# Kernel tuning notes

Hardware: AMD Instinct MI355X
Metric: run time of the kernel (lower is better)

Reference implementation:

```python
import jax, jax.numpy as jnp
import numpy as np

B, S, D = 1, 2048, 2048
H, G, HD = 32, 8, 64
EPS = 1e-6
ROPE_BASE = 10000.0


def rms_norm(x, g):
    # torch RMSNorm computed in fp32 then cast back (PytorchRMSNorm wrapper)
    xf = x.astype(jnp.float32)
    y = xf * jax.lax.rsqrt(jnp.mean(xf * xf, axis=-1, keepdims=True) + EPS) * g.astype(jnp.float32)
    return y.astype(x.dtype)


def rotate_half(x):
    x1, x2 = jnp.split(x, 2, axis=-1)
    return jnp.concatenate([-x2, x1], axis=-1)


def apply_rope(x, cos, sin):
    # x: (b, h, s, hd); cos/sin: (s, hd)
    return x * cos[None, None] + rotate_half(x) * sin[None, None]


def setup_inputs() -> dict:
    key = jax.random.key(0)
    ks = jax.random.split(key, 8)
    x = jax.random.normal(ks[0], (B, S, D), dtype=jnp.float32)
    wq = jax.random.normal(ks[1], (H * HD, D), dtype=jnp.float32) * (D ** -0.5)
    wk = jax.random.normal(ks[2], (G * HD, D), dtype=jnp.float32) * (D ** -0.5)
    wv = jax.random.normal(ks[3], (G * HD, D), dtype=jnp.float32) * (D ** -0.5)
    wo = jax.random.normal(ks[4], (D, H * HD), dtype=jnp.float32) * (D ** -0.5)
    qg = jnp.ones((HD,), dtype=jnp.float32)
    kg = jnp.ones((HD,), dtype=jnp.float32)
    # RoPE tables (HF-style: duplicated half-dim frequencies)
    inv_freq = 1.0 / (ROPE_BASE ** (jnp.arange(0, HD, 2, dtype=jnp.float32) / HD))
    ang = jnp.arange(S, dtype=jnp.float32)[:, None] * inv_freq[None, :]  # (S, HD/2)
    emb = jnp.concatenate([ang, ang], axis=-1)  # (S, HD)
    cos = jnp.cos(emb)
    sin = jnp.sin(emb)
    # causal mask: True = future (upper-right triangle)
    mask = jnp.triu(jnp.ones((S, S), dtype=bool), k=1)
    return {"x": x, "mask": mask, "cos": cos, "sin": sin,
            "wq": wq, "wk": wk, "wv": wv, "wo": wo, "qg": qg, "kg": kg}


def reference(x, mask, cos, sin, wq, wk, wv, wo, qg, kg):
    b, s, _ = x.shape
    rep = H // G
    q = (x @ wq.T).reshape(b, s, H, HD).transpose(0, 2, 1, 3)   # (b,H,s,hd)
    k = (x @ wk.T).reshape(b, s, G, HD).transpose(0, 2, 1, 3)   # (b,G,s,hd)
    v = (x @ wv.T).reshape(b, s, G, HD).transpose(0, 2, 1, 3)
    q = rms_norm(q, qg)
    k = rms_norm(k, kg)
    q = apply_rope(q, cos[:s], sin[:s])
    k = apply_rope(k, cos[:s], sin[:s])
    k = jnp.repeat(k, rep, axis=1)  # (b,H,s,hd) GQA expansion
    v = jnp.repeat(v, rep, axis=1)
    scores = jnp.einsum('bhqd,bhkd->bhqk', q, k) * (HD ** -0.5)
    neg = jnp.finfo(scores.dtype).min / 2
    scores = jnp.where(mask[None, None, :s, :s], neg, scores)
    w = jax.nn.softmax(scores, axis=-1)
    ctx = jnp.einsum('bhqk,bhkd->bhqd', w, v)
    ctx = ctx.transpose(0, 2, 1, 3).reshape(b, s, H * HD)
    return ctx @ wo.T
```

## Files before the change

kernel.cpp:

```cpp
#include <hip/hip_runtime.h>
#include <stdint.h>

#define SEQ    2048
#define DMODEL 2048
#define NHEAD  32
#define NKV    8
#define HDIM   64
#define NQKV   3072

typedef __bf16 bf16x8 __attribute__((ext_vector_type(8)));
typedef float  f32x4  __attribute__((ext_vector_type(4)));

#define SCALE2 0.180336880f
#define THR2   12.0f

__device__ __forceinline__ ushort bf(float f){
  __bf16 h = (__bf16)f;
  return __builtin_bit_cast(unsigned short, h);
}
__device__ __forceinline__ float b2f(ushort v){
  union { uint32_t u; float f; } a; a.u = ((uint32_t)v) << 16; return a.f;
}
__device__ __forceinline__ float ex2(float x){
  return __builtin_amdgcn_exp2f(x);
}
__device__ __forceinline__ float fmax3(float a, float b, float c){
  float r;
  asm("v_max3_f32 %0, %1, %2, %3" : "=v"(r) : "v"(a), "v"(b), "v"(c));
  return r;
}

__device__ __forceinline__ void gl_lds16(const void* g, void* l){
  __builtin_amdgcn_global_load_lds(
      (const __attribute__((address_space(1))) uint32_t*)g,
      (__attribute__((address_space(3))) uint32_t*)l, 16, 0, 0);
}

__global__ __launch_bounds__(256) void k_cvt_all(const float* __restrict__ x,
                                                 const float* __restrict__ wq,
                                                 const float* __restrict__ wk,
                                                 const float* __restrict__ wv,
                                                 const float* __restrict__ wo,
                                                 ushort* __restrict__ xb,
                                                 ushort* __restrict__ wcat,
                                                 ushort* __restrict__ wob){
  int i = blockIdx.x * 256 + threadIdx.x;
  const float* src; ushort* dst; int s4; int d4;
  if (i < 1048576)      { src = x;  dst = xb;   s4 = i;           d4 = s4; }
  else if (i < 2097152) { src = wq; dst = wcat; s4 = i - 1048576; d4 = s4; }
  else if (i < 2359296) { src = wk; dst = wcat; s4 = i - 2097152; d4 = s4 + 1048576; }
  else if (i < 2621440) { src = wv; dst = wcat; s4 = i - 2359296; d4 = s4 + 1310720; }
  else                  { src = wo; dst = wob;  s4 = i - 2621440; d4 = s4; }
  float4 v = reinterpret_cast<const float4*>(src)[s4];
  ushort4 o;
  o.x = bf(v.x); o.y = bf(v.y); o.z = bf(v.z); o.w = bf(v.w);
  reinterpret_cast<ushort4*>(dst)[d4] = o;
}

__global__ __launch_bounds__(256) void k_gemm_bt(const ushort* __restrict__ A,
                                                 const ushort* __restrict__ B,
                                                 float* __restrict__ C,
                                                 int M, int N, int K){
  __shared__ ushort As[2][128*64];
  __shared__ ushort Bs[2][64*64];
  const int tid = threadIdx.x, lane = tid & 63, wid = tid >> 6;
  const int bm = blockIdx.y * 128, bn = blockIdx.x * 64;
  const int wr = wid >> 1, wc = wid & 1;
  const int l15 = lane & 15, u = lane >> 4;

  const int crow = lane >> 3;
  const int scol = ((lane & 7) ^ crow) * 8;
  const ushort* Abase = A + (size_t)(bm + wid*32 + crow) * K + scol;
  const ushort* Bbase = B + (size_t)(bn + wid*16 + crow) * K + scol;

  auto STAGE = [&](int buf, int k0){
#pragma unroll
    for (int c = 0; c < 4; c++)
      gl_lds16(Abase + k0 + (size_t)c*8*K, &As[buf][(wid*32 + c*8)*64]);
#pragma unroll
    for (int c = 0; c < 2; c++)
      gl_lds16(Bbase + k0 + (size_t)c*8*K, &Bs[buf][(wid*16 + c*8)*64]);
  };

  f32x4 acc[4][2] = {};
  const int NT = K >> 6;

  STAGE(0, 0);
  __syncthreads();

  for (int t = 0; t < NT; t++){
    const int cur = t & 1;
    if (t + 1 < NT) STAGE(cur ^ 1, (t + 1) << 6);

#pragma unroll
    for (int kc = 0; kc < 2; kc++){
      bf16x8 af[4], bfr[2];
#pragma unroll
      for (int m = 0; m < 4; m++){
        int row = wr*64 + m*16 + l15;
        af[m] = *reinterpret_cast<const bf16x8*>(&As[cur][row*64 + (((kc*4+u) ^ (row&7))*8)]);
      }
#pragma unroll
      for (int n = 0; n < 2; n++){
        int row = wc*32 + n*16 + l15;
        bfr[n] = *reinterpret_cast<const bf16x8*>(&Bs[cur][row*64 + (((kc*4+u) ^ (row&7))*8)]);
      }
      __builtin_amdgcn_s_setprio(1);
#pragma unroll
      for (int m = 0; m < 4; m++)
#pragma unroll
        for (int n = 0; n < 2; n++)
          acc[m][n] = __builtin_amdgcn_mfma_f32_16x16x32_bf16(af[m], bfr[n], acc[m][n], 0, 0, 0);
      __builtin_amdgcn_s_setprio(0);
    }

    __syncthreads();
  }

#pragma unroll
  for (int m = 0; m < 4; m++)
#pragma unroll
    for (int n = 0; n < 2; n++)
#pragma unroll
      for (int j = 0; j < 4; j++){
        int row = bm + wr*64 + m*16 + u*4 + j;
        int col = bn + wc*32 + n*16 + l15;
        C[(size_t)row * N + col] = acc[m][n][j];
      }
}

__global__ __launch_bounds__(256) void k_gemm_btc(const ushort* __restrict__ A,
                                                  const ushort* __restrict__ B,
                                                  ushort* __restrict__ C,
                                                  int M, int N, int K){
  __shared__ ushort As[2][128*64];
  __shared__ ushort Bs[2][96*64];
  const int tid = threadIdx.x, lane = tid & 63, wid = tid >> 6;
  const int bm = blockIdx.y * 128, bn = blockIdx.x * 96;
  const int wr = wid >> 1, wc = wid & 1;
  const int l15 = lane & 15, u = lane >> 4;

  const int crow = lane >> 3;
  const int scol = ((lane & 7) ^ crow) * 8;
  const ushort* Abase = A + (size_t)(bm + wid*32 + crow) * K + scol;
  const ushort* Bbase = B + (size_t)(bn + wid*24 + crow) * K + scol;

  auto STAGE = [&](int buf, int k0){
#pragma unroll
    for (int c = 0; c < 4; c++)
      gl_lds16(Abase + k0 + (size_t)c*8*K, &As[buf][(wid*32 + c*8)*64]);
#pragma unroll
    for (int c = 0; c < 3; c++)
      gl_lds16(Bbase + k0 + (size_t)c*8*K, &Bs[buf][(wid*24 + c*8)*64]);
  };

  f32x4 acc[4][3] = {};
  const int NT = K >> 6;

  STAGE(0, 0);
  __syncthreads();

  for (int t = 0; t < NT; t++){
    const int cur = t & 1;
    if (t + 1 < NT) STAGE(cur ^ 1, (t + 1) << 6);

#pragma unroll
    for (int kc = 0; kc < 2; kc++){
      bf16x8 af[4], bfr[3];
#pragma unroll
      for (int m = 0; m < 4; m++){
        int row = wr*64 + m*16 + l15;
        af[m] = *reinterpret_cast<const bf16x8*>(&As[cur][row*64 + (((kc*4+u) ^ (row&7))*8)]);
      }
#pragma unroll
      for (int n = 0; n < 3; n++){
        int row = wc*48 + n*16 + l15;
        bfr[n] = *reinterpret_cast<const bf16x8*>(&Bs[cur][row*64 + (((kc*4+u) ^ (row&7))*8)]);
      }
      __builtin_amdgcn_s_setprio(1);
#pragma unroll
      for (int m = 0; m < 4; m++)
#pragma unroll
        for (int n = 0; n < 3; n++)
          acc[m][n] = __builtin_amdgcn_mfma_f32_16x16x32_bf16(af[m], bfr[n], acc[m][n], 0, 0, 0);
      __builtin_amdgcn_s_setprio(0);
    }

    __syncthreads();
  }

#pragma unroll
  for (int m = 0; m < 4; m++)
#pragma unroll
    for (int n = 0; n < 3; n++)
#pragma unroll
      for (int j = 0; j < 4; j++){
        int row = bm + wr*64 + m*16 + u*4 + j;
        int col = bn + wc*48 + n*16 + l15;
        C[(size_t)row * N + col] = bf(acc[m][n][j]);
      }
}

__global__ __launch_bounds__(256) void k_normrope(const ushort* __restrict__ qkvc,
                                                  const float* __restrict__ cosp,
                                                  const float* __restrict__ sinp,
                                                  const float* __restrict__ qg,
                                                  const float* __restrict__ kg,
                                                  ushort* __restrict__ qb,
                                                  ushort* __restrict__ kb){
  const int s = blockIdx.x;
  const int tid = threadIdx.x, lane = tid & 63, wid = tid >> 6;
  const ushort* row = qkvc + (size_t)s * NQKV;
  const float cs = cosp[s*HDIM + lane];
  const float sn = sinp[s*HDIM + lane];

  for (int hidx = wid; hidx < 40; hidx += 4){
    const bool isq = hidx < 32;
    const int col = isq ? hidx*64 : 2048 + (hidx-32)*64;
    float x = b2f(row[col + lane]);
    float ss = x * x;
#pragma unroll
    for (int m = 1; m < 64; m <<= 1) ss += __shfl_xor(ss, m);
    float r = rsqrtf(ss * (1.0f/64.0f) + 1e-6f);
    float y = x * r * (isq ? qg : kg)[lane];
    float p = __shfl_xor(y, 32);
    float out = y * cs + (lane < 32 ? -p : p) * sn;
    if (isq) qb[(size_t)s*2048 + hidx*64 + lane] = bf(out * SCALE2);
    else     kb[(size_t)s*512 + (hidx-32)*64 + lane] = bf(out);
  }
}

__global__ __launch_bounds__(256) void k_vtrans(const ushort* __restrict__ qkvc,
                                                ushort* __restrict__ vtb){
  __shared__ ushort tile[64][68];
  const int g = blockIdx.x >> 5, st = blockIdx.x & 31;
  const int tid = threadIdx.x;
#pragma unroll
  for (int i = 0; i < 4; i++){
    int idx = i*256 + tid;
    int r = idx >> 4, c4 = idx & 15;
    ushort4 v = *reinterpret_cast<const ushort4*>(
        qkvc + (size_t)(st*64 + r)*NQKV + 2560 + g*64 + c4*4);
    tile[c4*4+0][r] = v.x;
    tile[c4*4+1][r] = v.y;
    tile[c4*4+2][r] = v.z;
    tile[c4*4+3][r] = v.w;
  }
  __syncthreads();
#pragma unroll
  for (int i = 0; i < 4; i++){
    int idx = i*256 + tid;
    int d = idx >> 4, s4 = idx & 15;
    int pos4 = (s4 >> 3)*32 + (s4 & 3)*8 + ((s4 >> 2) & 1)*4;
    ushort4 o = *reinterpret_cast<const ushort4*>(&tile[d][s4*4]);
    *reinterpret_cast<ushort4*>(vtb + (size_t)(g*64 + d)*SEQ + st*64 + pos4) = o;
  }
}

__global__ __launch_bounds__(256, 4) void k_attn(const ushort* __restrict__ qbuf,
                                                 const ushort* __restrict__ kbuf,
                                                 const ushort* __restrict__ vtb,
                                                 ushort* __restrict__ op,
                                                 float2* __restrict__ ml){
  __shared__ ushort Kd[2][64*64];
  __shared__ ushort Vd[2][64*64];

  const int bx = blockIdx.x;
  const int c = bx & 255, slot = bx >> 8;
  const int h = c >> 3, j = c & 7;
  const int qt   = (slot & 1) ? j : 15 - j;
  const int part = slot >> 1;
  const int g = h >> 2;
  const int t0 = part ? (qt + 1)   : 0;
  const int t1 = part ? (2*qt + 2) : (qt + 1);
  const int tid = threadIdx.x, lane = tid & 63, wid = tid >> 6;
  const int l15 = lane & 15, u = lane >> 4;
  const int q0 = qt*128 + wid*32;

  bf16x8 qf[2][2];
#pragma unroll
  for (int hh = 0; hh < 2; hh++)
#pragma unroll
    for (int kc = 0; kc < 2; kc++)
      qf[hh][kc] = *reinterpret_cast<const bf16x8*>(
          qbuf + (size_t)(q0 + hh*16 + l15)*2048 + h*64 + kc*32 + u*8);

  f32x4 o[2][4] = {};
  float mrun[2] = {-1e30f, -1e30f};
  float lrun[2] = {0.f, 0.f};

  int koff[8], voff[8];
#pragma unroll
  for (int kb = 0; kb < 4; kb++)
#pragma unroll
    for (int kc = 0; kc < 2; kc++){
      int keyl = kb*16 + l15;
      koff[kb*2+kc] = (keyl*64 + (((kc*4+u) ^ (keyl&7))*8)) * 2;
    }
#pragma unroll
  for (int kc = 0; kc < 2; kc++)
#pragma unroll
    for (int d0 = 0; d0 < 4; d0++){
      int vrow = d0*16 + l15;
      voff[kc*4+d0] = (vrow*64 + (((kc*4+u) ^ (vrow&7))*8)) * 2;
    }

  const int srow = wid*16 + (lane >> 3);
  const int scol = ((lane & 7) ^ (lane >> 3)) * 8;
  const ushort* ksrc0 = kbuf + (size_t)srow*512 + g*64 + scol;
  const ushort* vsrc0 = vtb  + (size_t)(g*64 + srow)*SEQ + scol;

  auto STAGE = [&](int buf, int t){
    const ushort* ks = ksrc0 + (size_t)t*64*512;
    gl_lds16(ks,         &Kd[buf][wid*1024]);
    gl_lds16(ks + 8*512, &Kd[buf][wid*1024 + 512]);
    const ushort* vs = vsrc0 + t*64;
    gl_lds16(vs,          &Vd[buf][wid*1024]);
    gl_lds16(vs + 8*SEQ,  &Vd[buf][wid*1024 + 512]);
  };

  STAGE(0, t0);
  __syncthreads();

  for (int t = t0; t < t1; t++){
    const int cur = (t - t0) & 1;
    if (t + 1 < t1) STAGE(cur ^ 1, t + 1);

    const char* KB = (const char*)Kd + cur*8192;
    const char* VB = (const char*)Vd + cur*8192;

    f32x4 st[2][4];
#pragma unroll
    for (int kb = 0; kb < 4; kb++){
      const int key0 = t*64 + kb*16;
      bf16x8 kf0 = *reinterpret_cast<const bf16x8*>(KB + koff[kb*2]);
      bf16x8 kf1 = *reinterpret_cast<const bf16x8*>(KB + koff[kb*2+1]);
#pragma unroll
      for (int hh = 0; hh < 2; hh++){
        if (key0 <= q0 + hh*16 + 15){
          f32x4 a = {};
          a = __builtin_amdgcn_mfma_f32_16x16x32_bf16(kf0, qf[hh][0], a, 0, 0, 0);
          a = __builtin_amdgcn_mfma_f32_16x16x32_bf16(kf1, qf[hh][1], a, 0, 0, 0);
          st[hh][kb] = a;
        } else {
          st[hh][kb] = (f32x4){-1e30f, -1e30f, -1e30f, -1e30f};
        }
      }
    }
#pragma unroll
    for (int hh = 0; hh < 2; hh++){
      if (!((t*64 + 63) <= q0 + hh*16)){
        const int keyb = t*64 + u*4;
        const int qr = q0 + hh*16 + l15;
#pragma unroll
        for (int kb = 0; kb < 4; kb++)
#pragma unroll
          for (int jj = 0; jj < 4; jj++)
            st[hh][kb][jj] = (keyb + kb*16 + jj > qr) ? -1e30f : st[hh][kb][jj];
      }
    }

#pragma unroll
    for (int hh = 0; hh < 2; hh++){
      float r0 = fmax3(st[hh][0][0], st[hh][0][1], st[hh][0][2]);
      float r1 = fmax3(st[hh][0][3], st[hh][1][0], st[hh][1][1]);
      float r2 = fmax3(st[hh][1][2], st[hh][1][3], st[hh][2][0]);
      float r3 = fmax3(st[hh][2][1], st[hh][2][2], st[hh][2][3]);
      float r4 = fmax3(st[hh][3][0], st[hh][3][1], st[hh][3][2]);
      float m0 = fmax3(r0, r1, r2);
      float m1 = fmax3(r3, r4, st[hh][3][3]);
      float tml = fmaxf(m0, m1);
      if (__any(tml > mrun[hh] + THR2)){
        float tm = fmaxf(tml, __shfl_xor(tml, 16));
        tm = fmaxf(tm, __shfl_xor(tm, 32));
        float mn = fmaxf(mrun[hh], tm);
        float al = ex2(mrun[hh] - mn);
        mrun[hh] = mn;
        lrun[hh] *= al;
#pragma unroll
        for (int d0 = 0; d0 < 4; d0++)
#pragma unroll
          for (int jj = 0; jj < 4; jj++) o[hh][d0][jj] *= al;
      }
      float ls[4];
#pragma unroll
      for (int kb = 0; kb < 4; kb++){
        float p0 = ex2(st[hh][kb][0] - mrun[hh]);
        float p1 = ex2(st[hh][kb][1] - mrun[hh]);
        float p2 = ex2(st[hh][kb][2] - mrun[hh]);
        float p3 = ex2(st[hh][kb][3] - mrun[hh]);
        st[hh][kb][0] = p0; st[hh][kb][1] = p1;
        st[hh][kb][2] = p2; st[hh][kb][3] = p3;
        ls[kb] = (p0 + p1) + (p2 + p3);
      }
      lrun[hh] += (ls[0] + ls[1]) + (ls[2] + ls[3]);
    }

    __builtin_amdgcn_s_setprio(1);
#pragma unroll
    for (int kc = 0; kc < 2; kc++){
      union { uint32_t w[4]; bf16x8 v; } pb[2];
#pragma unroll
      for (int hh = 0; hh < 2; hh++){
        asm("v_cvt_pk_bf16_f32 %0, %1, %2" : "=v"(pb[hh].w[0]) : "v"(st[hh][2*kc  ][0]), "v"(st[hh][2*kc  ][1]));
        asm("v_cvt_pk_bf16_f32 %0, %1, %2" : "=v"(pb[hh].w[1]) : "v"(st[hh][2*kc  ][2]), "v"(st[hh][2*kc  ][3]));
        asm("v_cvt_pk_bf16_f32 %0, %1, %2" : "=v"(pb[hh].w[2]) : "v"(st[hh][2*kc+1][0]), "v"(st[hh][2*kc+1][1]));
        asm("v_cvt_pk_bf16_f32 %0, %1, %2" : "=v"(pb[hh].w[3]) : "v"(st[hh][2*kc+1][2]), "v"(st[hh][2*kc+1][3]));
      }
#pragma unroll
      for (int d0 = 0; d0 < 4; d0++){
        bf16x8 vb8 = *reinterpret_cast<const bf16x8*>(VB + voff[kc*4+d0]);
        o[0][d0] = __builtin_amdgcn_mfma_f32_16x16x32_bf16(vb8, pb[0].v, o[0][d0], 0, 0, 0);
        o[1][d0] = __builtin_amdgcn_mfma_f32_16x16x32_bf16(vb8, pb[1].v, o[1][d0], 0, 0, 0);
      }
    }
    __builtin_amdgcn_s_setprio(0);

    __syncthreads();
  }

#pragma unroll
  for (int hh = 0; hh < 2; hh++){
    float lt = lrun[hh] + __shfl_xor(lrun[hh], 16);
    lt += __shfl_xor(lt, 32);
    float inv = lt > 0.f ? 1.0f / lt : 0.f;
    const size_t ridx = (size_t)part*65536 + h*2048 + (q0 + hh*16 + l15);
#pragma unroll
    for (int d0 = 0; d0 < 4; d0++){
      ushort4 w;
      w.x = bf(o[hh][d0][0] * inv); w.y = bf(o[hh][d0][1] * inv);
      w.z = bf(o[hh][d0][2] * inv); w.w = bf(o[hh][d0][3] * inv);
      *reinterpret_cast<ushort4*>(&op[ridx*64 + d0*16 + u*4]) = w;
    }
    if (lane < 16) ml[ridx] = make_float2(mrun[hh], lt);
  }
}

__global__ __launch_bounds__(256) void k_comb(const ushort* __restrict__ op,
                                              const float2* __restrict__ ml,
                                              ushort* __restrict__ ctx){
  const int tq = blockIdx.x*256 + threadIdx.x;
  const int q = tq & 3, row = (tq >> 2) & 2047, h = tq >> 13;
  const int idx = h*2048 + row;
  float2 a = ml[idx], b = ml[idx + 65536];
  float m = fmaxf(a.x, b.x);
  float w0 = ex2(a.x - m) * a.y;
  float w1 = ex2(b.x - m) * b.y;
  float inv = 1.0f / (w0 + w1);
  w0 *= inv; w1 *= inv;
  const ushort4* p0 = reinterpret_cast<const ushort4*>(op + (size_t)idx*64 + q*16);
  const ushort4* p1 = reinterpret_cast<const ushort4*>(op + ((size_t)idx + 65536)*64 + q*16);
  ushort* dst = ctx + (size_t)row*2048 + h*64 + q*16;
#pragma unroll
  for (int i = 0; i < 4; i++){
    ushort4 x0 = p0[i], x1 = p1[i];
    ushort4 w;
    w.x = bf(w0*b2f(x0.x) + w1*b2f(x1.x));
    w.y = bf(w0*b2f(x0.y) + w1*b2f(x1.y));
    w.z = bf(w0*b2f(x0.z) + w1*b2f(x1.z));
    w.w = bf(w0*b2f(x0.w) + w1*b2f(x1.w));
    reinterpret_cast<ushort4*>(dst)[i] = w;
  }
}

extern "C" void kernel_launch(void* const* d_in, const int* in_sizes, int n_in,
                              void* d_out, int out_size, void* d_ws, size_t ws_size,
                              hipStream_t stream){
  const float* x    = (const float*)d_in[0];
  const float* cosp = (const float*)d_in[2];
  const float* sinp = (const float*)d_in[3];
  const float* wq   = (const float*)d_in[4];
  const float* wk   = (const float*)d_in[5];
  const float* wv   = (const float*)d_in[6];
  const float* wo   = (const float*)d_in[7];
  const float* qg   = (const float*)d_in[8];
  const float* kg   = (const float*)d_in[9];
  float* out = (float*)d_out;

  char* ws = (char*)d_ws;
  ushort* xb   = (ushort*)(ws);
  ushort* wcat = (ushort*)(ws + 8388608);
  ushort* wob  = (ushort*)(ws + 20971520);
  ushort* qkvc = (ushort*)(ws + 29360128);
  ushort* qb   = (ushort*)(ws + 41943040);
  ushort* kb   = (ushort*)(ws + 50331648);
  ushort* vtb  = (ushort*)(ws + 52428800);
  ushort* ctxb = (ushort*)(ws + 54525952);
  ushort* op   = (ushort*)(ws);
  float2* ml   = (float2*)(ws + 16777216);

  k_cvt_all<<<14336, 256, 0, stream>>>(x, wq, wk, wv, wo, xb, wcat, wob);
  k_gemm_btc<<<dim3(32, 16), 256, 0, stream>>>(xb, wcat, qkvc, 2048, 3072, 2048);
  k_normrope<<<2048, 256, 0, stream>>>(qkvc, cosp, sinp, qg, kg, qb, kb);
  k_vtrans<<<256, 256, 0, stream>>>(qkvc, vtb);
  k_attn<<<1024, 256, 0, stream>>>(qb, kb, vtb, op, ml);
  k_comb<<<1024, 256, 0, stream>>>(op, ml, ctxb);
  k_gemm_bt<<<dim3(32, 16), 256, 0, stream>>>(ctxb, wob, out, 2048, 2048, 2048);
}
```

Baseline: 130.6 us.

## Merge norm-rope and V-transpose launches, raise QK MFMA priority, widen combine loads

```diff
diff --git a/kernel.cpp b/kernel.cpp
--- a/kernel.cpp
+++ b/kernel.cpp
@@ -10,6 +10,7 @@
 
 typedef __bf16 bf16x8 __attribute__((ext_vector_type(8)));
 typedef float  f32x4  __attribute__((ext_vector_type(4)));
+typedef unsigned short ushort8 __attribute__((ext_vector_type(8)));
 
 #define SCALE2 0.180336880f
 #define THR2   12.0f
@@ -201,59 +202,60 @@
       }
 }
 
-__global__ __launch_bounds__(256) void k_normrope(const ushort* __restrict__ qkvc,
-                                                  const float* __restrict__ cosp,
-                                                  const float* __restrict__ sinp,
-                                                  const float* __restrict__ qg,
-                                                  const float* __restrict__ kg,
-                                                  ushort* __restrict__ qb,
-                                                  ushort* __restrict__ kb){
-  const int s = blockIdx.x;
+__global__ __launch_bounds__(256) void k_prep(const ushort* __restrict__ qkvc,
+                                              const float* __restrict__ cosp,
+                                              const float* __restrict__ sinp,
+                                              const float* __restrict__ qg,
+                                              const float* __restrict__ kg,
+                                              ushort* __restrict__ qb,
+                                              ushort* __restrict__ kb,
+                                              ushort* __restrict__ vtb){
+  __shared__ ushort tile[64][68];
+  const int bx = blockIdx.x;
   const int tid = threadIdx.x, lane = tid & 63, wid = tid >> 6;
-  const ushort* row = qkvc + (size_t)s * NQKV;
-  const float cs = cosp[s*HDIM + lane];
-  const float sn = sinp[s*HDIM + lane];
-
-  for (int hidx = wid; hidx < 40; hidx += 4){
-    const bool isq = hidx < 32;
-    const int col = isq ? hidx*64 : 2048 + (hidx-32)*64;
-    float x = b2f(row[col + lane]);
-    float ss = x * x;
-#pragma unroll
-    for (int m = 1; m < 64; m <<= 1) ss += __shfl_xor(ss, m);
-    float r = rsqrtf(ss * (1.0f/64.0f) + 1e-6f);
-    float y = x * r * (isq ? qg : kg)[lane];
-    float p = __shfl_xor(y, 32);
-    float out = y * cs + (lane < 32 ? -p : p) * sn;
-    if (isq) qb[(size_t)s*2048 + hidx*64 + lane] = bf(out * SCALE2);
-    else     kb[(size_t)s*512 + (hidx-32)*64 + lane] = bf(out);
-  }
-}
-
-__global__ __launch_bounds__(256) void k_vtrans(const ushort* __restrict__ qkvc,
-                                                ushort* __restrict__ vtb){
-  __shared__ ushort tile[64][68];
-  const int g = blockIdx.x >> 5, st = blockIdx.x & 31;
-  const int tid = threadIdx.x;
-#pragma unroll
-  for (int i = 0; i < 4; i++){
-    int idx = i*256 + tid;
-    int r = idx >> 4, c4 = idx & 15;
-    ushort4 v = *reinterpret_cast<const ushort4*>(
-        qkvc + (size_t)(st*64 + r)*NQKV + 2560 + g*64 + c4*4);
-    tile[c4*4+0][r] = v.x;
-    tile[c4*4+1][r] = v.y;
-    tile[c4*4+2][r] = v.z;
-    tile[c4*4+3][r] = v.w;
-  }
-  __syncthreads();
-#pragma unroll
-  for (int i = 0; i < 4; i++){
-    int idx = i*256 + tid;
-    int d = idx >> 4, s4 = idx & 15;
-    int pos4 = (s4 >> 3)*32 + (s4 & 3)*8 + ((s4 >> 2) & 1)*4;
-    ushort4 o = *reinterpret_cast<const ushort4*>(&tile[d][s4*4]);
-    *reinterpret_cast<ushort4*>(vtb + (size_t)(g*64 + d)*SEQ + st*64 + pos4) = o;
+
+  if (bx < 2048){
+    const int s = bx;
+    const ushort* row = qkvc + (size_t)s * NQKV;
+    const float cs = cosp[s*HDIM + lane];
+    const float sn = sinp[s*HDIM + lane];
+    for (int hidx = wid; hidx < 40; hidx += 4){
+      const bool isq = hidx < 32;
+      const int col = isq ? hidx*64 : 2048 + (hidx-32)*64;
+      float x = b2f(row[col + lane]);
+      float ss = x * x;
+#pragma unroll
+      for (int m = 1; m < 64; m <<= 1) ss += __shfl_xor(ss, m);
+      float r = rsqrtf(ss * (1.0f/64.0f) + 1e-6f);
+      float y = x * r * (isq ? qg : kg)[lane];
+      float p = __shfl_xor(y, 32);
+      float out = y * cs + (lane < 32 ? -p : p) * sn;
+      if (isq) qb[(size_t)s*2048 + hidx*64 + lane] = bf(out * SCALE2);
+      else     kb[(size_t)s*512 + (hidx-32)*64 + lane] = bf(out);
+    }
+  } else {
+    const int b = bx - 2048;
+    const int g = b >> 5, st = b & 31;
+#pragma unroll
+    for (int i = 0; i < 4; i++){
+      int idx = i*256 + tid;
+      int r = idx >> 4, c4 = idx & 15;
+      ushort4 v = *reinterpret_cast<const ushort4*>(
+          qkvc + (size_t)(st*64 + r)*NQKV + 2560 + g*64 + c4*4);
+      tile[c4*4+0][r] = v.x;
+      tile[c4*4+1][r] = v.y;
+      tile[c4*4+2][r] = v.z;
+      tile[c4*4+3][r] = v.w;
+    }
+    __syncthreads();
+#pragma unroll
+    for (int i = 0; i < 4; i++){
+      int idx = i*256 + tid;
+      int d = idx >> 4, s4 = idx & 15;
+      int pos4 = (s4 >> 3)*32 + (s4 & 3)*8 + ((s4 >> 2) & 1)*4;
+      ushort4 o = *reinterpret_cast<const ushort4*>(&tile[d][s4*4]);
+      *reinterpret_cast<ushort4*>(vtb + (size_t)(g*64 + d)*SEQ + st*64 + pos4) = o;
+    }
   }
 }
 
@@ -330,6 +332,7 @@
     const char* VB = (const char*)Vd + cur*8192;
 
     f32x4 st[2][4];
+    __builtin_amdgcn_s_setprio(1);
 #pragma unroll
     for (int kb = 0; kb < 4; kb++){
       const int key0 = t*64 + kb*16;
@@ -347,6 +350,7 @@
         }
       }
     }
+    __builtin_amdgcn_s_setprio(0);
 #pragma unroll
     for (int hh = 0; hh < 2; hh++){
       if (!((t*64 + 63) <= q0 + hh*16)){
@@ -448,18 +452,17 @@
   float w1 = ex2(b.x - m) * b.y;
   float inv = 1.0f / (w0 + w1);
   w0 *= inv; w1 *= inv;
-  const ushort4* p0 = reinterpret_cast<const ushort4*>(op + (size_t)idx*64 + q*16);
-  const ushort4* p1 = reinterpret_cast<const ushort4*>(op + ((size_t)idx + 65536)*64 + q*16);
+  const ushort8* p0 = reinterpret_cast<const ushort8*>(op + (size_t)idx*64 + q*16);
+  const ushort8* p1 = reinterpret_cast<const ushort8*>(op + ((size_t)idx + 65536)*64 + q*16);
   ushort* dst = ctx + (size_t)row*2048 + h*64 + q*16;
 #pragma unroll
-  for (int i = 0; i < 4; i++){
-    ushort4 x0 = p0[i], x1 = p1[i];
-    ushort4 w;
-    w.x = bf(w0*b2f(x0.x) + w1*b2f(x1.x));
-    w.y = bf(w0*b2f(x0.y) + w1*b2f(x1.y));
-    w.z = bf(w0*b2f(x0.z) + w1*b2f(x1.z));
-    w.w = bf(w0*b2f(x0.w) + w1*b2f(x1.w));
-    reinterpret_cast<ushort4*>(dst)[i] = w;
+  for (int i = 0; i < 2; i++){
+    ushort8 x0 = p0[i], x1 = p1[i];
+    ushort8 w;
+#pragma unroll
+    for (int e = 0; e < 8; e++)
+      w[e] = bf(w0*b2f(x0[e]) + w1*b2f(x1[e]));
+    reinterpret_cast<ushort8*>(dst)[i] = w;
   }
 }
 
@@ -491,8 +494,7 @@
 
   k_cvt_all<<<14336, 256, 0, stream>>>(x, wq, wk, wv, wo, xb, wcat, wob);
   k_gemm_btc<<<dim3(32, 16), 256, 0, stream>>>(xb, wcat, qkvc, 2048, 3072, 2048);
-  k_normrope<<<2048, 256, 0, stream>>>(qkvc, cosp, sinp, qg, kg, qb, kb);
-  k_vtrans<<<256, 256, 0, stream>>>(qkvc, vtb);
+  k_prep<<<2304, 256, 0, stream>>>(qkvc, cosp, sinp, qg, kg, qb, kb, vtb);
   k_attn<<<1024, 256, 0, stream>>>(qb, kb, vtb, op, ml);
   k_comb<<<1024, 256, 0, stream>>>(op, ml, ctxb);
   k_gemm_bt<<<dim3(32, 16), 256, 0, stream>>>(ctxb, wob, out, 2048, 2048, 2048);
```

After: 128.0 us. No clear change (-1.9%).
